# Optimization experiments

Hardware: AMD Instinct MI355X
Metric: run time of the kernel (lower is better)

The kernel has to match this reference:

```python
import jax, jax.numpy as jnp
import numpy as np

# AWQ packing: nibble for unpacked column j (within a packed int32 of 8 values)
# lives at bit offset 4 * AWQ_ORDER[j]  (the 'reverse AWQ order').
AWQ_ORDER = (0, 4, 1, 5, 2, 6, 3, 7)
GROUP_SIZE = 128


def _unpack_int4(packed):
    """[R, C] int32 -> [R, 8*C] int32 of 4-bit values in AWQ order."""
    shifts = jnp.array(AWQ_ORDER, dtype=jnp.int32) * 4  # [8]
    nib = jnp.right_shift(packed[:, :, None], shifts) & 0xF  # [R, C, 8]
    return nib.reshape(packed.shape[0], -1)


def setup_inputs() -> dict:
    key = jax.random.key(0)
    k1, k2, k3, k4 = jax.random.split(key, 4)
    M, K, N = 1024, 4096, 11008
    G = K // GROUP_SIZE  # 32
    x = jax.random.normal(k1, (M, K), dtype=jnp.float32)
    imin = jnp.iinfo(jnp.int32).min
    imax = jnp.iinfo(jnp.int32).max
    qweight = jax.random.randint(k2, (K, N // 8), imin, imax, dtype=jnp.int32)
    qzeros = jax.random.randint(k3, (G, N // 8), imin, imax, dtype=jnp.int32)
    scales = jax.random.uniform(k4, (G, N), dtype=jnp.float32, minval=0.001, maxval=0.01)
    return {"x": x, "qweight": qweight, "scales": scales, "qzeros": qzeros}


def reference(x, qweight, scales, qzeros):
    # Dequantize: W[k, n] = (w4[k, n] - z4[k//gs, n]) * scales[k//gs, n]
    K = qweight.shape[0]
    gs = K // qzeros.shape[0]  # group size
    w4 = _unpack_int4(qweight).astype(jnp.float32)   # [K, N]
    z4 = _unpack_int4(qzeros).astype(jnp.float32)    # [G, N]
    z = jnp.repeat(z4, gs, axis=0)                   # [K, N]
    s = jnp.repeat(scales, gs, axis=0)               # [K, N]
    W = (w4 - z) * s                                 # [K, N]
    # FP16_MATMUL_HEURISTIC path: dequantize then plain matmul
    return jnp.matmul(x, W)                          # [M, N]
```

## Files before the change

### kernel.cpp

```cpp
#include <hip/hip_runtime.h>
#include <stdint.h>

#define M_DIM 1024
#define K_DIM 4096
#define N_DIM 11008
#define NC_DIM 1376
#define G_DIM 32
#define GS 128

typedef __bf16 bf16x8 __attribute__((ext_vector_type(8)));
typedef float f32x4 __attribute__((ext_vector_type(4)));
typedef unsigned short ushort8 __attribute__((ext_vector_type(8)));

typedef __attribute__((address_space(1))) char as1_char;
typedef __attribute__((address_space(3))) char as3_char;
#define GLDS16(g, l) __builtin_amdgcn_global_load_lds((as1_char*)(g), (as3_char*)(l), 16, 0, 0)

static __device__ __forceinline__ int awq_shift(int j) {
  return ((j & 1) << 4) | ((j >> 1) << 2);
}

static __device__ __forceinline__ unsigned short f2bf(float f) {
  union { float f; uint32_t u; } c; c.f = f;
  uint32_t u = c.u;
  return (unsigned short)((u + 0x7FFFu + ((u >> 16) & 1u)) >> 16);
}

__global__ void k_cvt_x(const float* __restrict__ x, unsigned short* __restrict__ xb) {
  int i = blockIdx.x * blockDim.x + threadIdx.x;
  int base = i * 8;
  float4 v0 = *(const float4*)(x + base);
  float4 v1 = *(const float4*)(x + base + 4);
  ushort8 o;
  o[0] = f2bf(v0.x); o[1] = f2bf(v0.y); o[2] = f2bf(v0.z); o[3] = f2bf(v0.w);
  o[4] = f2bf(v1.x); o[5] = f2bf(v1.y); o[6] = f2bf(v1.z); o[7] = f2bf(v1.w);
  *(ushort8*)(xb + base) = o;
}

__global__ void k_dequant(const int* __restrict__ qw, const float* __restrict__ scales,
                          const int* __restrict__ qz, unsigned short* __restrict__ wt,
                          int n_base) {
  __shared__ int wlds[64][17];
  const int t = threadIdx.x;
  const int k0 = blockIdx.x * 64;
  const int nb = blockIdx.y;
  const int n_glob0 = n_base + nb * 128;
  const int c0 = n_glob0 >> 3;
  const int g = k0 >> 7;
#pragma unroll
  for (int p = 0; p < 4; ++p) {
    int idx = p * 256 + t;
    int k = idx >> 4, c = idx & 15;
    wlds[k][c] = qw[(size_t)(k0 + k) * NC_DIM + c0 + c];
  }
  __syncthreads();
#pragma unroll
  for (int p = 0; p < 4; ++p) {
    int u = p * 256 + t;
    int k8 = u & 7;
    int nl = u >> 3;
    int j = nl & 7;
    int c = nl >> 3;
    int shift = awq_shift(j);
    float s = scales[(size_t)g * N_DIM + n_glob0 + nl];
    int zw = qz[(size_t)g * NC_DIM + c0 + c];
    float zs = (float)((zw >> shift) & 0xF) * s;
    ushort8 o;
#pragma unroll
    for (int i = 0; i < 8; ++i) {
      int wv = wlds[k8 * 8 + i][c];
      int nib = (wv >> shift) & 0xF;
      o[i] = f2bf(fmaf((float)nib, s, -zs));
    }
    *(ushort8*)(wt + (size_t)(nb * 128 + nl) * K_DIM + k0 + k8 * 8) = o;
  }
}

__launch_bounds__(256, 2)
__global__ void k_gemm(const unsigned short* __restrict__ A,
                       const unsigned short* __restrict__ Bt,
                       float* __restrict__ C, int n_base) {
  __shared__ unsigned short As[128 * 32];
  __shared__ unsigned short Bs[128 * 32];
  const int tid = threadIdx.x;
  const int lane = tid & 63;
  const int w = tid >> 6;
  const int wr = w >> 1, wc = w & 1;
  const int m0 = blockIdx.x * 128;
  const int nb0 = blockIdx.y * 128;
  const int lrow = lane >> 2;
  const int lk = lane & 3;

  f32x4 acc[4][4] = {};

  const size_t a_row0 = (size_t)(m0 + w * 32) * K_DIM;
  const size_t b_row0 = (size_t)(nb0 + w * 32) * K_DIM;

  for (int kt = 0; kt < K_DIM / 32; ++kt) {
    const int k0 = kt * 32;
#pragma unroll
    for (int i = 0; i < 2; ++i) {
      const unsigned short* ga = A + a_row0 + (size_t)(i * 16 + lrow) * K_DIM + k0 + lk * 8;
      GLDS16(ga, &As[(w * 32 + i * 16) * 32]);
      const unsigned short* gb = Bt + b_row0 + (size_t)(i * 16 + lrow) * K_DIM + k0 + lk * 8;
      GLDS16(gb, &Bs[(w * 32 + i * 16) * 32]);
    }
    __syncthreads();

    bf16x8 af[4], bfr[4];
#pragma unroll
    for (int mi = 0; mi < 4; ++mi)
      af[mi] = *(const bf16x8*)&As[(wr * 64 + mi * 16 + (lane & 15)) * 32 + (lane >> 4) * 8];
#pragma unroll
    for (int ni = 0; ni < 4; ++ni)
      bfr[ni] = *(const bf16x8*)&Bs[(wc * 64 + ni * 16 + (lane & 15)) * 32 + (lane >> 4) * 8];
#pragma unroll
    for (int mi = 0; mi < 4; ++mi)
#pragma unroll
      for (int ni = 0; ni < 4; ++ni)
        acc[mi][ni] = __builtin_amdgcn_mfma_f32_16x16x32_bf16(af[mi], bfr[ni], acc[mi][ni], 0, 0, 0);
    __syncthreads();
  }

  const int crow_base = m0 + wr * 64 + (lane >> 4) * 4;
  const int ccol = n_base + nb0 + wc * 64 + (lane & 15);
#pragma unroll
  for (int mi = 0; mi < 4; ++mi)
#pragma unroll
    for (int ni = 0; ni < 4; ++ni)
#pragma unroll
      for (int r = 0; r < 4; ++r)
        C[(size_t)(crow_base + mi * 16 + r) * N_DIM + ccol + ni * 16] = acc[mi][ni][r];
}

__global__ void k_fallback(const float* __restrict__ x, const int* __restrict__ qw,
                           const float* __restrict__ scales, const int* __restrict__ qz,
                           float* __restrict__ C) {
  int t = blockIdx.x * 256 + threadIdx.x;
  int m = t / NC_DIM;
  int c = t % NC_DIM;
  float acc[8];
#pragma unroll
  for (int j = 0; j < 8; ++j) acc[j] = 0.f;
  for (int g = 0; g < G_DIM; ++g) {
    int zw = qz[(size_t)g * NC_DIM + c];
    float sj[8], zsj[8];
#pragma unroll
    for (int j = 0; j < 8; ++j) {
      int shift = awq_shift(j);
      sj[j] = scales[(size_t)g * N_DIM + c * 8 + j];
      zsj[j] = (float)((zw >> shift) & 0xF) * sj[j];
    }
    for (int k = g * GS; k < (g + 1) * GS; ++k) {
      float xv = x[(size_t)m * K_DIM + k];
      int wv = qw[(size_t)k * NC_DIM + c];
#pragma unroll
      for (int j = 0; j < 8; ++j) {
        float dq = fmaf((float)((wv >> awq_shift(j)) & 0xF), sj[j], -zsj[j]);
        acc[j] = fmaf(xv, dq, acc[j]);
      }
    }
  }
#pragma unroll
  for (int j = 0; j < 8; ++j)
    C[(size_t)m * N_DIM + c * 8 + j] = acc[j];
}

extern "C" void kernel_launch(void* const* d_in, const int* in_sizes, int n_in,
                              void* d_out, int out_size, void* d_ws, size_t ws_size,
                              hipStream_t stream) {
  (void)in_sizes; (void)n_in; (void)out_size;
  const float* x = (const float*)d_in[0];
  const int* qw = (const int*)d_in[1];
  const float* scales = (const float*)d_in[2];
  const int* qz = (const int*)d_in[3];
  float* C = (float*)d_out;

  const size_t xb_bytes = (size_t)M_DIM * K_DIM * 2;
  size_t avail = ws_size > xb_bytes ? ws_size - xb_bytes : 0;
  int nc_cols = (int)(avail / ((size_t)K_DIM * 2));
  int nchunk = (nc_cols / 128) * 128;
  if (nchunk > N_DIM) nchunk = N_DIM;

  if (nchunk >= 128) {
    unsigned short* xb = (unsigned short*)d_ws;
    unsigned short* wt = (unsigned short*)((char*)d_ws + xb_bytes);
    k_cvt_x<<<(M_DIM * K_DIM) / (256 * 8), 256, 0, stream>>>(x, xb);
    for (int n_base = 0; n_base < N_DIM; n_base += nchunk) {
      int cur = N_DIM - n_base; if (cur > nchunk) cur = nchunk;
      dim3 gd(K_DIM / 64, cur / 128);
      k_dequant<<<gd, 256, 0, stream>>>(qw, scales, qz, wt, n_base);
      dim3 gg(M_DIM / 128, cur / 128);
      k_gemm<<<gg, 256, 0, stream>>>(xb, wt, C, n_base);
    }
  } else {
    k_fallback<<<(M_DIM * NC_DIM) / 256, 256, 0, stream>>>(x, qw, scales, qz, C);
  }
}
```

Measured before the change: 160.2 us.

## Replace GEMM with 256x256 double-buffered, swizzled 8-wave MFMA kernel

Replaces the simple 128x128 single-buffered BK=32 GEMM with a 512-thread kernel that computes 256x256 output tiles using BK=64. The kernel double-buffers A and B in 128KB of LDS, applies an XOR swizzle, and interleaves staged global-to-LDS loads with MFMA phases using s_setprio. Blocks are remapped across XCDs for cache locality. The N-chunking loop is dropped and the whole weight is dequantized in one launch, which requires a workspace large enough for the full bf16 weight. Only 172 blocks are launched, so some CUs may sit idle.

```diff
diff --git a/kernel.cpp b/kernel.cpp
--- a/kernel.cpp
+++ b/kernel.cpp
@@ -38,13 +38,12 @@
 }
 
 __global__ void k_dequant(const int* __restrict__ qw, const float* __restrict__ scales,
-                          const int* __restrict__ qz, unsigned short* __restrict__ wt,
-                          int n_base) {
+                          const int* __restrict__ qz, unsigned short* __restrict__ wt) {
   __shared__ int wlds[64][17];
   const int t = threadIdx.x;
   const int k0 = blockIdx.x * 64;
   const int nb = blockIdx.y;
-  const int n_glob0 = n_base + nb * 128;
+  const int n_glob0 = nb * 128;
   const int c0 = n_glob0 >> 3;
   const int g = k0 >> 7;
 #pragma unroll
@@ -76,61 +75,157 @@
   }
 }
 
-__launch_bounds__(256, 2)
-__global__ void k_gemm(const unsigned short* __restrict__ A,
-                       const unsigned short* __restrict__ Bt,
-                       float* __restrict__ C, int n_base) {
-  __shared__ unsigned short As[128 * 32];
-  __shared__ unsigned short Bs[128 * 32];
+#define BK 64
+#define NT (K_DIM / BK)
+#define REG_BYTES 16384
+
+__device__ __forceinline__ void stage_half(const unsigned short* __restrict__ src, int row0, int T,
+                                           unsigned char* lds_region, int w, int lane) {
+  const int kb = (((lane & 7) ^ ((lane >> 3) & 7)) << 4);
+  const int row = w * 16 + (lane >> 3);
+  const unsigned short* g = src + (size_t)(row0 + row) * K_DIM + T * 64 + (kb >> 1);
+  unsigned char* l = lds_region + w * 2048;
+  GLDS16(g, l);
+  GLDS16(g + (size_t)8 * K_DIM, l + 1024);
+}
+
+#define RD(base, off) (*(const bf16x8*)((const unsigned char*)(base) + (off)))
+#define MFMA16(a, b, c) __builtin_amdgcn_mfma_f32_16x16x32_bf16((a), (b), (c), 0, 0, 0)
+
+__launch_bounds__(512, 2)
+__global__ void k_gemm8(const unsigned short* __restrict__ A,
+                        const unsigned short* __restrict__ Bt,
+                        float* __restrict__ C) {
+  __shared__ __attribute__((aligned(16))) unsigned char LDS[131072];
+
   const int tid = threadIdx.x;
   const int lane = tid & 63;
   const int w = tid >> 6;
-  const int wr = w >> 1, wc = w & 1;
-  const int m0 = blockIdx.x * 128;
-  const int nb0 = blockIdx.y * 128;
-  const int lrow = lane >> 2;
-  const int lk = lane & 3;
-
-  f32x4 acc[4][4] = {};
-
-  const size_t a_row0 = (size_t)(m0 + w * 32) * K_DIM;
-  const size_t b_row0 = (size_t)(nb0 + w * 32) * K_DIM;
-
-  for (int kt = 0; kt < K_DIM / 32; ++kt) {
-    const int k0 = kt * 32;
-#pragma unroll
-    for (int i = 0; i < 2; ++i) {
-      const unsigned short* ga = A + a_row0 + (size_t)(i * 16 + lrow) * K_DIM + k0 + lk * 8;
-      GLDS16(ga, &As[(w * 32 + i * 16) * 32]);
-      const unsigned short* gb = Bt + b_row0 + (size_t)(i * 16 + lrow) * K_DIM + k0 + lk * 8;
-      GLDS16(gb, &Bs[(w * 32 + i * 16) * 32]);
-    }
-    __syncthreads();
-
-    bf16x8 af[4], bfr[4];
-#pragma unroll
-    for (int mi = 0; mi < 4; ++mi)
-      af[mi] = *(const bf16x8*)&As[(wr * 64 + mi * 16 + (lane & 15)) * 32 + (lane >> 4) * 8];
-#pragma unroll
-    for (int ni = 0; ni < 4; ++ni)
-      bfr[ni] = *(const bf16x8*)&Bs[(wc * 64 + ni * 16 + (lane & 15)) * 32 + (lane >> 4) * 8];
-#pragma unroll
-    for (int mi = 0; mi < 4; ++mi)
-#pragma unroll
-      for (int ni = 0; ni < 4; ++ni)
-        acc[mi][ni] = __builtin_amdgcn_mfma_f32_16x16x32_bf16(af[mi], bfr[ni], acc[mi][ni], 0, 0, 0);
-    __syncthreads();
-  }
-
-  const int crow_base = m0 + wr * 64 + (lane >> 4) * 4;
-  const int ccol = n_base + nb0 + wc * 64 + (lane & 15);
-#pragma unroll
-  for (int mi = 0; mi < 4; ++mi)
-#pragma unroll
-    for (int ni = 0; ni < 4; ++ni)
+  const int wm = w >> 2;
+  const int wn = w & 3;
+  const int u = lane & 15;
+  const int h = lane >> 4;
+  const int xor16 = (lane & 7) << 4;
+  const int kpos0 = (h * 16) ^ xor16;
+  const int kpos1 = (64 + h * 16) ^ xor16;
+  const int aoff = u * 128;
+
+  const int orig = blockIdx.x;
+  const int xcd = orig & 7, loc = orig >> 3;
+  const int qq = 21, rr = 4;
+  const int swz = (xcd < rr) ? xcd * (qq + 1) + loc : rr * (qq + 1) + (xcd - rr) * qq + loc;
+  const int m0 = (swz & 3) * 256;
+  const int nb0 = (swz >> 2) * 256;
+
+  f32x4 acc[8][4] = {};
+
+  stage_half(A,  m0,        0, LDS + 0 * REG_BYTES, w, lane);
+  stage_half(A,  m0 + 128,  0, LDS + 1 * REG_BYTES, w, lane);
+  stage_half(Bt, nb0,       0, LDS + 2 * REG_BYTES, w, lane);
+  stage_half(Bt, nb0 + 128, 0, LDS + 3 * REG_BYTES, w, lane);
+  stage_half(Bt, nb0,       1, LDS + 65536 + 2 * REG_BYTES, w, lane);
+  stage_half(A,  m0,        1, LDS + 65536 + 0 * REG_BYTES, w, lane);
+  asm volatile("s_waitcnt vmcnt(4)" ::: "memory");
+  __builtin_amdgcn_s_barrier();
+
+#pragma unroll 2
+  for (int t = 0; t < NT; ++t) {
+    const int cur = t & 1;
+    unsigned char* bufc = LDS + cur * 65536;
+    unsigned char* bufn = LDS + (cur ^ 1) * 65536;
+    const unsigned char* rA = bufc + wm * REG_BYTES;
+    const unsigned char* rB = bufc + (2 + (wn >> 1)) * REG_BYTES;
+    const int bsub = (wn & 1) * 8192;
+
+    bf16x8 aR[4][2], bLo[2][2], bHi[2][2];
+
+#pragma unroll
+    for (int mi = 0; mi < 4; ++mi) {
+      aR[mi][0] = RD(rA, mi * 2048 + aoff + kpos0);
+      aR[mi][1] = RD(rA, mi * 2048 + aoff + kpos1);
+    }
+#pragma unroll
+    for (int nf = 0; nf < 2; ++nf) {
+      bLo[nf][0] = RD(rB, bsub + nf * 2048 + aoff + kpos0);
+      bLo[nf][1] = RD(rB, bsub + nf * 2048 + aoff + kpos1);
+    }
+    if (t + 1 < NT) stage_half(A, m0 + 128, t + 1, bufn + 1 * REG_BYTES, w, lane);
+    __builtin_amdgcn_s_barrier();
+    __builtin_amdgcn_s_setprio(1);
+#pragma unroll
+    for (int mi = 0; mi < 4; ++mi)
+#pragma unroll
+      for (int nf = 0; nf < 2; ++nf) {
+        acc[mi][nf] = MFMA16(aR[mi][0], bLo[nf][0], acc[mi][nf]);
+        acc[mi][nf] = MFMA16(aR[mi][1], bLo[nf][1], acc[mi][nf]);
+      }
+    __builtin_amdgcn_s_setprio(0);
+    __builtin_amdgcn_s_barrier();
+
+#pragma unroll
+    for (int nf = 0; nf < 2; ++nf) {
+      bHi[nf][0] = RD(rB, bsub + (nf + 2) * 2048 + aoff + kpos0);
+      bHi[nf][1] = RD(rB, bsub + (nf + 2) * 2048 + aoff + kpos1);
+    }
+    if (t + 1 < NT) stage_half(Bt, nb0 + 128, t + 1, bufn + 3 * REG_BYTES, w, lane);
+    __builtin_amdgcn_s_barrier();
+    __builtin_amdgcn_s_setprio(1);
+#pragma unroll
+    for (int mi = 0; mi < 4; ++mi)
+#pragma unroll
+      for (int nf = 0; nf < 2; ++nf) {
+        acc[mi][nf + 2] = MFMA16(aR[mi][0], bHi[nf][0], acc[mi][nf + 2]);
+        acc[mi][nf + 2] = MFMA16(aR[mi][1], bHi[nf][1], acc[mi][nf + 2]);
+      }
+    __builtin_amdgcn_s_setprio(0);
+    __builtin_amdgcn_s_barrier();
+
+#pragma unroll
+    for (int mi = 0; mi < 4; ++mi) {
+      aR[mi][0] = RD(rA, (mi + 4) * 2048 + aoff + kpos0);
+      aR[mi][1] = RD(rA, (mi + 4) * 2048 + aoff + kpos1);
+    }
+    if (t + 2 < NT) stage_half(Bt, nb0, t + 2, bufc + 2 * REG_BYTES, w, lane);
+    __builtin_amdgcn_s_barrier();
+    __builtin_amdgcn_s_setprio(1);
+#pragma unroll
+    for (int mi = 0; mi < 4; ++mi)
+#pragma unroll
+      for (int nf = 0; nf < 2; ++nf) {
+        acc[mi + 4][nf + 2] = MFMA16(aR[mi][0], bHi[nf][0], acc[mi + 4][nf + 2]);
+        acc[mi + 4][nf + 2] = MFMA16(aR[mi][1], bHi[nf][1], acc[mi + 4][nf + 2]);
+      }
+    __builtin_amdgcn_s_setprio(0);
+    __builtin_amdgcn_s_barrier();
+
+    if (t + 2 < NT) stage_half(A, m0, t + 2, bufc + 0 * REG_BYTES, w, lane);
+    __builtin_amdgcn_s_barrier();
+    __builtin_amdgcn_s_setprio(1);
+#pragma unroll
+    for (int mi = 0; mi < 4; ++mi)
+#pragma unroll
+      for (int nf = 0; nf < 2; ++nf) {
+        acc[mi + 4][nf] = MFMA16(aR[mi][0], bLo[nf][0], acc[mi + 4][nf]);
+        acc[mi + 4][nf] = MFMA16(aR[mi][1], bLo[nf][1], acc[mi + 4][nf]);
+      }
+    __builtin_amdgcn_s_setprio(0);
+    if (t < NT - 2) {
+      asm volatile("s_waitcnt vmcnt(4)" ::: "memory");
+    } else {
+      asm volatile("s_waitcnt vmcnt(0)" ::: "memory");
+    }
+    __builtin_amdgcn_s_barrier();
+  }
+
+  const int crow0 = m0 + wm * 128 + h * 4;
+  const int ccol0 = nb0 + wn * 64 + u;
+#pragma unroll
+  for (int mi = 0; mi < 8; ++mi)
+#pragma unroll
+    for (int nf = 0; nf < 4; ++nf)
 #pragma unroll
       for (int r = 0; r < 4; ++r)
-        C[(size_t)(crow_base + mi * 16 + r) * N_DIM + ccol + ni * 16] = acc[mi][ni][r];
+        C[(size_t)(crow0 + mi * 16 + r) * N_DIM + ccol0 + nf * 16] = acc[mi][nf][r];
 }
 
 __global__ void k_fallback(const float* __restrict__ x, const int* __restrict__ qw,
@@ -147,9 +242,8 @@
     float sj[8], zsj[8];
 #pragma unroll
     for (int j = 0; j < 8; ++j) {
-      int shift = awq_shift(j);
       sj[j] = scales[(size_t)g * N_DIM + c * 8 + j];
-      zsj[j] = (float)((zw >> shift) & 0xF) * sj[j];
+      zsj[j] = (float)((zw >> awq_shift(j)) & 0xF) * sj[j];
     }
     for (int k = g * GS; k < (g + 1) * GS; ++k) {
       float xv = x[(size_t)m * K_DIM + k];
@@ -177,22 +271,15 @@
   float* C = (float*)d_out;
 
   const size_t xb_bytes = (size_t)M_DIM * K_DIM * 2;
-  size_t avail = ws_size > xb_bytes ? ws_size - xb_bytes : 0;
-  int nc_cols = (int)(avail / ((size_t)K_DIM * 2));
-  int nchunk = (nc_cols / 128) * 128;
-  if (nchunk > N_DIM) nchunk = N_DIM;
-
-  if (nchunk >= 128) {
+  const size_t wt_bytes = (size_t)N_DIM * K_DIM * 2;
+
+  if (ws_size >= xb_bytes + wt_bytes) {
     unsigned short* xb = (unsigned short*)d_ws;
     unsigned short* wt = (unsigned short*)((char*)d_ws + xb_bytes);
     k_cvt_x<<<(M_DIM * K_DIM) / (256 * 8), 256, 0, stream>>>(x, xb);
-    for (int n_base = 0; n_base < N_DIM; n_base += nchunk) {
-      int cur = N_DIM - n_base; if (cur > nchunk) cur = nchunk;
-      dim3 gd(K_DIM / 64, cur / 128);
-      k_dequant<<<gd, 256, 0, stream>>>(qw, scales, qz, wt, n_base);
-      dim3 gg(M_DIM / 128, cur / 128);
-      k_gemm<<<gg, 256, 0, stream>>>(xb, wt, C, n_base);
-    }
+    dim3 gd(K_DIM / 64, N_DIM / 128);
+    k_dequant<<<gd, 256, 0, stream>>>(qw, scales, qz, wt);
+    k_gemm8<<<(M_DIM / 256) * (N_DIM / 256), 512, 0, stream>>>(xb, wt, C);
   } else {
     k_fallback<<<(M_DIM * NC_DIM) / 256, 256, 0, stream>>>(x, qw, scales, qz, C);
   }
```

Result: faster. 131.3 us, median of 2 (-18.0%).
